# Performance work log

Measured on AMD Instinct MI355X. Metric: run time of the kernel, lower is better.

Reference implementation:

```python
import jax, jax.numpy as jnp
import numpy as np

N = 1024      # nodes == subgraphs (NGNN: one subgraph per node)
DEG = 8       # average degree
E = N * DEG   # edges
IND = 32      # indim
OUTD = 32     # outdim


def setup_inputs() -> dict:
    key = jax.random.key(0)
    k0, k1, k2, k3, k4 = jax.random.split(key, 5)
    X = jax.random.normal(k0, (N, N, IND), dtype=jnp.float32)
    # binary tuple-support mask (which (i,j) tuples exist in the sparse 2D tensor)
    mask = jax.random.randint(k1, (N, N), 0, 2).astype(jnp.int32)
    # adjacency edge list: A[row, col] = 1 (structure-only sparse adjacency)
    edge_row = jax.random.randint(k2, (E,), 0, N)  # destination j
    edge_col = jax.random.randint(k3, (E,), 0, N)  # source k
    # MLP (single linear layer, PygHO MLP default)
    W = jax.random.normal(k4, (IND, OUTD), dtype=jnp.float32) / np.sqrt(IND).astype(np.float32)
    b = jnp.zeros((OUTD,), dtype=jnp.float32)
    return {"X": X, "mask": mask, "edge_row": edge_row, "edge_col": edge_col, "W": W, "b": b}


def reference(X, mask, edge_row, edge_col, W, b):
    n = X.shape[0]
    m = mask.astype(X.dtype)[..., None]                      # [n, n, 1]
    # tuplewise MLP on existing tuples: tX[i,j] = X[i,j] @ W + b
    tX = (jnp.einsum("ijd,de->ije", X, W) + b) * m           # [n, n, OUTD]
    # message passing within each subgraph i along node dim j:
    # ret[i, j] = sum_{k : A[j,k]=1} tX[i, k]
    msgs = jnp.take(tX, edge_col, axis=1)                    # [n, E, OUTD] gather sources
    msgs = jnp.moveaxis(msgs, 1, 0)                          # [E, n, OUTD]
    agg = jax.ops.segment_sum(msgs, edge_row, num_segments=n)  # [j, i, OUTD]
    ret = jnp.swapaxes(agg, 0, 1) * m                        # restrict to tuple support (tarX = tX)
    return ret
```

## Files before the change

kernel.cpp:

```cpp
#include <hip/hip_runtime.h>


#define NN   1024
#define IND  32
#define OUTD 32
#define EE   8192

typedef __attribute__((ext_vector_type(2))) float f32x2;

__global__ __launch_bounds__(1024) void k_zero(int* __restrict__ p, int n) {
    const int t = blockIdx.x * 1024 + threadIdx.x;
    if (t < n) p[t] = 0;
}

__global__ __launch_bounds__(1024) void k_count(const int* __restrict__ erow,
                                                int* __restrict__ cnt, int n_edges) {
    const int e = blockIdx.x * 1024 + threadIdx.x;
    if (e < n_edges) atomicAdd(&cnt[erow[e]], 1);
}

__global__ __launch_bounds__(1024) void k_scan(const int* __restrict__ cnt,
                                               int* __restrict__ row_ptr,
                                               int* __restrict__ fill) {
    __shared__ int sb[NN];
    const int t = threadIdx.x;
    const int v = cnt[t];
    sb[t] = v;
    __syncthreads();
    #pragma unroll
    for (int off = 1; off < NN; off <<= 1) {
        const int a = (t >= off) ? sb[t - off] : 0;
        __syncthreads();
        sb[t] += a;
        __syncthreads();
    }
    const int excl = sb[t] - v;
    row_ptr[t] = excl;
    fill[t]    = excl;
    if (t == NN - 1) row_ptr[NN] = sb[t];
}

__global__ __launch_bounds__(1024) void k_scatter(const int* __restrict__ erow,
                                                  const int* __restrict__ ecol,
                                                  int* __restrict__ fill,
                                                  int* __restrict__ cols, int n_edges) {
    const int e = blockIdx.x * 1024 + threadIdx.x;
    if (e < n_edges) {
        const int pos = atomicAdd(&fill[erow[e]], 1);
        cols[pos] = ecol[e];
    }
}

__global__ __launch_bounds__(1024) void ngnn_main_kernel(
    const float* __restrict__ X, const int* __restrict__ mask,
    const float* __restrict__ W, const float* __restrict__ b,
    const int* __restrict__ row_ptr, const int* __restrict__ cols,
    float* __restrict__ out, int n_edges)
{
    extern __shared__ float smem[];
    float* Xl    = smem;
    float* maskf = smem + NN * IND;
    unsigned short* colsl = (unsigned short*)(smem + NN * IND + NN);

    const int t = threadIdx.x;
    const int i = blockIdx.x;

    const float4* Xg = (const float4*)(X + (size_t)i * NN * IND);
    float4 xv[8];
    #pragma unroll
    for (int it = 0; it < 8; ++it) xv[it] = Xg[it * 1024 + t];

    int cv[8];
    #pragma unroll
    for (int it = 0; it < 8; ++it) {
        const int e = it * 1024 + t;
        cv[it] = (e < n_edges) ? cols[e] : 0;
    }

    const int j  = t;
    const int e0 = row_ptr[j];
    const int e1 = row_ptr[j + 1];

    maskf[t] = (float)mask[(size_t)i * NN + t];
    __syncthreads();

    #pragma unroll
    for (int it = 0; it < 8; ++it) {
        const int f4 = it * 1024 + t;
        const int k  = f4 >> 3;
        const int p  = (f4 & 7) ^ (k & 7);
        const float m = maskf[k];
        float4 v = xv[it];
        v.x *= m; v.y *= m; v.z *= m; v.w *= m;
        *(float4*)(Xl + (k << 5) + (p << 2)) = v;
    }
    #pragma unroll
    for (int it = 0; it < 8; ++it) {
        const int e = it * 1024 + t;
        if (e < n_edges && e < EE) {
            const int k = cv[it] & (NN - 1);
            colsl[e] = (unsigned short)(k | ((maskf[k] != 0.f) ? 1024 : 0));
        }
    }
    __syncthreads();

    const float mj = maskf[j];
    f32x2 o2[16];

    if (mj != 0.f) {
        float4 S4[8];
        #pragma unroll
        for (int s = 0; s < 8; ++s) S4[s] = make_float4(0.f, 0.f, 0.f, 0.f);
        int cnt = 0;

        for (int e = e0; e < e1; ++e) {
            const int c = (int)colsl[e];
            const int k = c & (NN - 1);
            cnt += c >> 10;
            const float* rb = Xl + (k << 5);
            const int kb = (k & 7) << 2;
            #pragma unroll
            for (int s = 0; s < 8; ++s) {
                const float4 v = *(const float4*)(rb + ((s << 2) ^ kb));
                S4[s].x += v.x; S4[s].y += v.y; S4[s].z += v.z; S4[s].w += v.w;
            }
        }

        float S[IND];
        #pragma unroll
        for (int s = 0; s < 8; ++s) {
            S[4*s+0] = S4[s].x; S[4*s+1] = S4[s].y;
            S[4*s+2] = S4[s].z; S[4*s+3] = S4[s].w;
        }

        const float cntf = (float)cnt;
        const f32x2* W2 = (const f32x2*)W;
        const f32x2* b2 = (const f32x2*)b;
        #pragma unroll
        for (int c = 0; c < 16; ++c) o2[c] = b2[c] * cntf;
        #pragma unroll
        for (int d = 0; d < IND; ++d) {
            const float s = S[d];
            #pragma unroll
            for (int c = 0; c < 16; ++c) o2[c] += W2[d * 16 + c] * s;
        }
    } else {
        #pragma unroll
        for (int c = 0; c < 16; ++c) { o2[c].x = 0.f; o2[c].y = 0.f; }
    }

    __syncthreads();
    #pragma unroll
    for (int q = 0; q < 8; ++q) {
        const int p = q ^ (j & 7);
        *(float4*)(Xl + (j << 5) + (p << 2)) =
            make_float4(o2[2*q].x, o2[2*q].y, o2[2*q+1].x, o2[2*q+1].y);
    }
    __syncthreads();
    float4* Og = (float4*)(out + (size_t)i * NN * IND);
    #pragma unroll
    for (int it = 0; it < 8; ++it) {
        const int f4 = it * 1024 + t;
        const int k  = f4 >> 3;
        const int p  = (f4 & 7) ^ (k & 7);
        Og[f4] = *(const float4*)(Xl + (k << 5) + (p << 2));
    }
}

extern "C" void kernel_launch(void* const* d_in, const int* in_sizes, int n_in,
                              void* d_out, int out_size, void* d_ws, size_t ws_size,
                              hipStream_t stream) {
    const float* X    = (const float*)d_in[0];
    const int*   mask = (const int*)d_in[1];
    const int*   erow = (const int*)d_in[2];
    const int*   ecol = (const int*)d_in[3];
    const float* W    = (const float*)d_in[4];
    const float* b    = (const float*)d_in[5];
    float*       out  = (float*)d_out;

    const int n_edges = in_sizes[2];

    int* cnt     = (int*)d_ws;
    int* row_ptr = cnt + 1024;
    int* fill    = cnt + 2560;
    int* cols    = cnt + 4096;

    const int eb = (n_edges + 1023) / 1024;
    k_zero   <<<1, 1024, 0, stream>>>(cnt, NN);
    k_count  <<<eb, 1024, 0, stream>>>(erow, cnt, n_edges);
    k_scan   <<<1, 1024, 0, stream>>>(cnt, row_ptr, fill);
    k_scatter<<<eb, 1024, 0, stream>>>(erow, ecol, fill, cols, n_edges);

    const size_t shmem = (size_t)NN * IND * sizeof(float)
                       + (size_t)NN * sizeof(float)
                       + (size_t)EE * sizeof(unsigned short);
    hipFuncSetAttribute((const void*)ngnn_main_kernel,
                        hipFuncAttributeMaxDynamicSharedMemorySize, (int)shmem);
    ngnn_main_kernel<<<NN, 1024, shmem, stream>>>(X, mask, W, b, row_ptr, cols, out, n_edges);
}
```

Before: 316.4 us.

## Fuse CSR construction into main kernel and process four subgraphs per block

Drops the four preprocessing launches (zero, count, scan, scatter) and builds the CSR adjacency in LDS inside each block with LDS atomics and a scan. Each block now handles four subgraphs in sequence, which spreads the CSR build cost over four subgraphs and prefetches the next subgraph's X and mask into registers while the current one is staged. Syncthreads are replaced by an explicit lgkmcnt wait plus barrier. In exchange, the grid shrinks to 256 blocks of 1024 threads, so there is less parallelism for hiding memory latency, and every block repeats the edge-list work. The mask flag bits are also rewritten into the shared column list on each iteration.

New measurement: 318.7 us. About the same (+0.7%).

```diff
diff --git a/kernel.cpp b/kernel.cpp
--- a/kernel.cpp
+++ b/kernel.cpp
@@ -8,162 +8,163 @@
 
 typedef __attribute__((ext_vector_type(2))) float f32x2;
 
-__global__ __launch_bounds__(1024) void k_zero(int* __restrict__ p, int n) {
-    const int t = blockIdx.x * 1024 + threadIdx.x;
-    if (t < n) p[t] = 0;
-}
+#define BARRIER_LDS() do { \
+    asm volatile("s_waitcnt lgkmcnt(0)" ::: "memory"); \
+    __builtin_amdgcn_s_barrier(); \
+} while (0)
 
-__global__ __launch_bounds__(1024) void k_count(const int* __restrict__ erow,
-                                                int* __restrict__ cnt, int n_edges) {
-    const int e = blockIdx.x * 1024 + threadIdx.x;
-    if (e < n_edges) atomicAdd(&cnt[erow[e]], 1);
-}
-
-__global__ __launch_bounds__(1024) void k_scan(const int* __restrict__ cnt,
-                                               int* __restrict__ row_ptr,
-                                               int* __restrict__ fill) {
-    __shared__ int sb[NN];
-    const int t = threadIdx.x;
-    const int v = cnt[t];
-    sb[t] = v;
-    __syncthreads();
-    #pragma unroll
-    for (int off = 1; off < NN; off <<= 1) {
-        const int a = (t >= off) ? sb[t - off] : 0;
-        __syncthreads();
-        sb[t] += a;
-        __syncthreads();
-    }
-    const int excl = sb[t] - v;
-    row_ptr[t] = excl;
-    fill[t]    = excl;
-    if (t == NN - 1) row_ptr[NN] = sb[t];
-}
-
-__global__ __launch_bounds__(1024) void k_scatter(const int* __restrict__ erow,
-                                                  const int* __restrict__ ecol,
-                                                  int* __restrict__ fill,
-                                                  int* __restrict__ cols, int n_edges) {
-    const int e = blockIdx.x * 1024 + threadIdx.x;
-    if (e < n_edges) {
-        const int pos = atomicAdd(&fill[erow[e]], 1);
-        cols[pos] = ecol[e];
-    }
-}
-
-__global__ __launch_bounds__(1024) void ngnn_main_kernel(
+__global__ __launch_bounds__(1024) void ngnn_fused_kernel(
     const float* __restrict__ X, const int* __restrict__ mask,
+    const int* __restrict__ erow, const int* __restrict__ ecol,
     const float* __restrict__ W, const float* __restrict__ b,
-    const int* __restrict__ row_ptr, const int* __restrict__ cols,
     float* __restrict__ out, int n_edges)
 {
     extern __shared__ float smem[];
-    float* Xl    = smem;
-    float* maskf = smem + NN * IND;
-    unsigned short* colsl = (unsigned short*)(smem + NN * IND + NN);
+    float*          Xl    = smem;
+    int*            rp    = (int*)(smem + NN * IND);
+    float*          maskf = (float*)(rp + NN + 1);
+    unsigned short* colsl = (unsigned short*)(maskf + NN);
 
-    const int t = threadIdx.x;
-    const int i = blockIdx.x;
+    const int t  = threadIdx.x;
+    const int i0 = blockIdx.x * 4;
 
-    const float4* Xg = (const float4*)(X + (size_t)i * NN * IND);
+    const float4* Xg = (const float4*)(X + (size_t)i0 * NN * IND);
     float4 xv[8];
     #pragma unroll
     for (int it = 0; it < 8; ++it) xv[it] = Xg[it * 1024 + t];
+    int mv = mask[(size_t)i0 * NN + t];
 
-    int cv[8];
+    int er[8], ec[8];
     #pragma unroll
     for (int it = 0; it < 8; ++it) {
         const int e = it * 1024 + t;
-        cv[it] = (e < n_edges) ? cols[e] : 0;
+        er[it] = (e < n_edges) ? (erow[e] & (NN - 1)) : -1;
+        ec[it] = (e < n_edges) ? (ecol[e] & (NN - 1)) : 0;
     }
 
-    const int j  = t;
-    const int e0 = row_ptr[j];
-    const int e1 = row_ptr[j + 1];
-
-    maskf[t] = (float)mask[(size_t)i * NN + t];
-    __syncthreads();
-
+    int* scnt = (int*)smem;
+    scnt[t] = 0;
+    BARRIER_LDS();
+    #pragma unroll
+    for (int it = 0; it < 8; ++it)
+        if (er[it] >= 0) atomicAdd(&scnt[er[it]], 1);
+    BARRIER_LDS();
+    const int myv = scnt[t];
+    for (int off = 1; off < NN; off <<= 1) {
+        const int a = (t >= off) ? scnt[t - off] : 0;
+        BARRIER_LDS();
+        scnt[t] += a;
+        BARRIER_LDS();
+    }
+    const int incl = scnt[t];
+    int* fill = (int*)maskf;
+    rp[t]   = incl - myv;
+    fill[t] = incl - myv;
+    if (t == NN - 1) rp[NN] = incl;
+    BARRIER_LDS();
+    const int e0 = rp[t];
+    const int e1 = rp[t + 1];
     #pragma unroll
     for (int it = 0; it < 8; ++it) {
-        const int f4 = it * 1024 + t;
-        const int k  = f4 >> 3;
-        const int p  = (f4 & 7) ^ (k & 7);
-        const float m = maskf[k];
-        float4 v = xv[it];
-        v.x *= m; v.y *= m; v.z *= m; v.w *= m;
-        *(float4*)(Xl + (k << 5) + (p << 2)) = v;
-    }
-    #pragma unroll
-    for (int it = 0; it < 8; ++it) {
-        const int e = it * 1024 + t;
-        if (e < n_edges && e < EE) {
-            const int k = cv[it] & (NN - 1);
-            colsl[e] = (unsigned short)(k | ((maskf[k] != 0.f) ? 1024 : 0));
+        if (er[it] >= 0) {
+            const int pos = atomicAdd(&fill[er[it]], 1);
+            colsl[pos] = (unsigned short)ec[it];
         }
     }
-    __syncthreads();
+    BARRIER_LDS();
 
-    const float mj = maskf[j];
-    f32x2 o2[16];
+    #pragma unroll 1
+    for (int r = 0; r < 4; ++r) {
+        const int i = i0 + r;
 
-    if (mj != 0.f) {
-        float4 S4[8];
+        maskf[t] = (float)mv;
+        BARRIER_LDS();
+
         #pragma unroll
-        for (int s = 0; s < 8; ++s) S4[s] = make_float4(0.f, 0.f, 0.f, 0.f);
-        int cnt = 0;
+        for (int it = 0; it < 8; ++it) {
+            const int f4 = it * 1024 + t;
+            const int k  = f4 >> 3;
+            const int p  = (f4 & 7) ^ (k & 7);
+            const float m = maskf[k];
+            float4 v = xv[it];
+            v.x *= m; v.y *= m; v.z *= m; v.w *= m;
+            *(float4*)(Xl + (k << 5) + (p << 2)) = v;
+        }
+        #pragma unroll
+        for (int it = 0; it < 8; ++it) {
+            const int e = it * 1024 + t;
+            if (e < n_edges) {
+                const int k = (int)colsl[e] & (NN - 1);
+                colsl[e] = (unsigned short)(k | ((maskf[k] != 0.f) ? 1024 : 0));
+            }
+        }
+        if (r < 3) {
+            const float4* Xgn = (const float4*)(X + (size_t)(i + 1) * NN * IND);
+            #pragma unroll
+            for (int it = 0; it < 8; ++it) xv[it] = Xgn[it * 1024 + t];
+            mv = mask[(size_t)(i + 1) * NN + t];
+        }
+        BARRIER_LDS();
 
-        for (int e = e0; e < e1; ++e) {
-            const int c = (int)colsl[e];
-            const int k = c & (NN - 1);
-            cnt += c >> 10;
-            const float* rb = Xl + (k << 5);
-            const int kb = (k & 7) << 2;
+        const float mj = maskf[t];
+        f32x2 o2[16];
+        if (mj != 0.f) {
+            float4 S4[8];
+            #pragma unroll
+            for (int s = 0; s < 8; ++s) S4[s] = make_float4(0.f, 0.f, 0.f, 0.f);
+            int cnt = 0;
+            for (int e = e0; e < e1; ++e) {
+                const int c = (int)colsl[e];
+                const int k = c & (NN - 1);
+                cnt += c >> 10;
+                const float* rb = Xl + (k << 5);
+                const int kb = (k & 7) << 2;
+                #pragma unroll
+                for (int s = 0; s < 8; ++s) {
+                    const float4 v = *(const float4*)(rb + ((s << 2) ^ kb));
+                    S4[s].x += v.x; S4[s].y += v.y; S4[s].z += v.z; S4[s].w += v.w;
+                }
+            }
+            float S[IND];
             #pragma unroll
             for (int s = 0; s < 8; ++s) {
-                const float4 v = *(const float4*)(rb + ((s << 2) ^ kb));
-                S4[s].x += v.x; S4[s].y += v.y; S4[s].z += v.z; S4[s].w += v.w;
+                S[4*s+0] = S4[s].x; S[4*s+1] = S4[s].y;
+                S[4*s+2] = S4[s].z; S[4*s+3] = S4[s].w;
             }
+            const float cntf = (float)cnt;
+            const f32x2* W2 = (const f32x2*)W;
+            const f32x2* b2 = (const f32x2*)b;
+            #pragma unroll
+            for (int c = 0; c < 16; ++c) o2[c] = b2[c] * cntf;
+            #pragma unroll
+            for (int d = 0; d < IND; ++d) {
+                const float s = S[d];
+                #pragma unroll
+                for (int c = 0; c < 16; ++c) o2[c] += W2[d * 16 + c] * s;
+            }
+        } else {
+            #pragma unroll
+            for (int c = 0; c < 16; ++c) { o2[c].x = 0.f; o2[c].y = 0.f; }
         }
+        BARRIER_LDS();
 
-        float S[IND];
         #pragma unroll
-        for (int s = 0; s < 8; ++s) {
-            S[4*s+0] = S4[s].x; S[4*s+1] = S4[s].y;
-            S[4*s+2] = S4[s].z; S[4*s+3] = S4[s].w;
+        for (int q = 0; q < 8; ++q) {
+            const int p = q ^ (t & 7);
+            *(float4*)(Xl + (t << 5) + (p << 2)) =
+                make_float4(o2[2*q].x, o2[2*q].y, o2[2*q+1].x, o2[2*q+1].y);
         }
+        BARRIER_LDS();
 
-        const float cntf = (float)cnt;
-        const f32x2* W2 = (const f32x2*)W;
-        const f32x2* b2 = (const f32x2*)b;
+        float4* Og = (float4*)(out + (size_t)i * NN * IND);
         #pragma unroll
-        for (int c = 0; c < 16; ++c) o2[c] = b2[c] * cntf;
-        #pragma unroll
-        for (int d = 0; d < IND; ++d) {
-            const float s = S[d];
-            #pragma unroll
-            for (int c = 0; c < 16; ++c) o2[c] += W2[d * 16 + c] * s;
+        for (int it = 0; it < 8; ++it) {
+            const int f4 = it * 1024 + t;
+            const int k  = f4 >> 3;
+            const int p  = (f4 & 7) ^ (k & 7);
+            Og[f4] = *(const float4*)(Xl + (k << 5) + (p << 2));
         }
-    } else {
-        #pragma unroll
-        for (int c = 0; c < 16; ++c) { o2[c].x = 0.f; o2[c].y = 0.f; }
-    }
-
-    __syncthreads();
-    #pragma unroll
-    for (int q = 0; q < 8; ++q) {
-        const int p = q ^ (j & 7);
-        *(float4*)(Xl + (j << 5) + (p << 2)) =
-            make_float4(o2[2*q].x, o2[2*q].y, o2[2*q+1].x, o2[2*q+1].y);
-    }
-    __syncthreads();
-    float4* Og = (float4*)(out + (size_t)i * NN * IND);
-    #pragma unroll
-    for (int it = 0; it < 8; ++it) {
-        const int f4 = it * 1024 + t;
-        const int k  = f4 >> 3;
-        const int p  = (f4 & 7) ^ (k & 7);
-        Og[f4] = *(const float4*)(Xl + (k << 5) + (p << 2));
+        BARRIER_LDS();
     }
 }
 
@@ -178,23 +179,14 @@
     const float* b    = (const float*)d_in[5];
     float*       out  = (float*)d_out;
 
-    const int n_edges = in_sizes[2];
-
-    int* cnt     = (int*)d_ws;
-    int* row_ptr = cnt + 1024;
-    int* fill    = cnt + 2560;
-    int* cols    = cnt + 4096;
-
-    const int eb = (n_edges + 1023) / 1024;
-    k_zero   <<<1, 1024, 0, stream>>>(cnt, NN);
-    k_count  <<<eb, 1024, 0, stream>>>(erow, cnt, n_edges);
-    k_scan   <<<1, 1024, 0, stream>>>(cnt, row_ptr, fill);
-    k_scatter<<<eb, 1024, 0, stream>>>(erow, ecol, fill, cols, n_edges);
+    int n_edges = in_sizes[2];
+    if (n_edges > EE) n_edges = EE;
 
     const size_t shmem = (size_t)NN * IND * sizeof(float)
+                       + (size_t)(NN + 1) * sizeof(int)
                        + (size_t)NN * sizeof(float)
                        + (size_t)EE * sizeof(unsigned short);
-    hipFuncSetAttribute((const void*)ngnn_main_kernel,
+    hipFuncSetAttribute((const void*)ngnn_fused_kernel,
                         hipFuncAttributeMaxDynamicSharedMemorySize, (int)shmem);
-    ngnn_main_kernel<<<NN, 1024, shmem, stream>>>(X, mask, W, b, row_ptr, cols, out, n_edges);
+    ngnn_fused_kernel<<<NN / 4, 1024, shmem, stream>>>(X, mask, erow, ecol, W, b, out, n_edges);
 }
```

## Skip masked rows and gather X directly from global instead of staging in LDS

Applied to the files above, without the earlier changes.

The main kernel no longer stages the whole X slice in shared memory. It builds a per-block compacted list of active destination rows and their masked source columns, then gathers source rows straight from global memory, so masked-out X rows are never read. Masked output rows are written as zeros, and the block shrinks to 256 threads with a much smaller LDS footprint, allowing several blocks per CU. The cost is uncoalesced, L2-dependent random row gathers in place of streaming loads, a per-block serial pass over the CSR, and an atomic-built active list that leaves load imbalance across threads.

New measurement: 335.9 us. 6.2% more time.

```diff
diff --git a/kernel.cpp b/kernel.cpp
--- a/kernel.cpp
+++ b/kernel.cpp
@@ -51,119 +51,98 @@
     }
 }
 
-__global__ __launch_bounds__(1024) void ngnn_main_kernel(
+__global__ __launch_bounds__(256, 4) void ngnn_main_kernel(
     const float* __restrict__ X, const int* __restrict__ mask,
     const float* __restrict__ W, const float* __restrict__ b,
     const int* __restrict__ row_ptr, const int* __restrict__ cols,
-    float* __restrict__ out, int n_edges)
+    float* __restrict__ out)
 {
-    extern __shared__ float smem[];
-    float* Xl    = smem;
-    float* maskf = smem + NN * IND;
-    unsigned short* colsl = (unsigned short*)(smem + NN * IND + NN);
+    __shared__ float          maskf[NN];
+    __shared__ unsigned int   meta[NN];
+    __shared__ unsigned short colsl[EE];
+    __shared__ unsigned short alist[NN];
+    __shared__ int            acount;
 
     const int t = threadIdx.x;
     const int i = blockIdx.x;
 
-    const float4* Xg = (const float4*)(X + (size_t)i * NN * IND);
-    float4 xv[8];
-    #pragma unroll
-    for (int it = 0; it < 8; ++it) xv[it] = Xg[it * 1024 + t];
-
-    int cv[8];
-    #pragma unroll
-    for (int it = 0; it < 8; ++it) {
-        const int e = it * 1024 + t;
-        cv[it] = (e < n_edges) ? cols[e] : 0;
+    if (t == 0) acount = 0;
+    {
+        const int4 m4 = ((const int4*)(mask + (size_t)i * NN))[t];
+        maskf[4*t+0] = (float)m4.x; maskf[4*t+1] = (float)m4.y;
+        maskf[4*t+2] = (float)m4.z; maskf[4*t+3] = (float)m4.w;
     }
-
-    const int j  = t;
-    const int e0 = row_ptr[j];
-    const int e1 = row_ptr[j + 1];
-
-    maskf[t] = (float)mask[(size_t)i * NN + t];
     __syncthreads();
 
     #pragma unroll
-    for (int it = 0; it < 8; ++it) {
-        const int f4 = it * 1024 + t;
-        const int k  = f4 >> 3;
-        const int p  = (f4 & 7) ^ (k & 7);
-        const float m = maskf[k];
-        float4 v = xv[it];
-        v.x *= m; v.y *= m; v.z *= m; v.w *= m;
-        *(float4*)(Xl + (k << 5) + (p << 2)) = v;
-    }
-    #pragma unroll
-    for (int it = 0; it < 8; ++it) {
-        const int e = it * 1024 + t;
-        if (e < n_edges && e < EE) {
-            const int k = cv[it] & (NN - 1);
-            colsl[e] = (unsigned short)(k | ((maskf[k] != 0.f) ? 1024 : 0));
+    for (int p = 0; p < 4; ++p) {
+        const int j = p * 256 + t;
+        if (maskf[j] != 0.f) {
+            const int a   = row_ptr[j];
+            const int bnd = row_ptr[j + 1];
+            int c = 0;
+            for (int e = a; e < bnd; ++e) {
+                const int k = cols[e] & (NN - 1);
+                if (maskf[k] != 0.f) colsl[a + (c++)] = (unsigned short)k;
+            }
+            meta[j] = (unsigned)a | ((unsigned)c << 16);
+            const int pos = atomicAdd(&acount, 1);
+            alist[pos] = (unsigned short)j;
         }
     }
     __syncthreads();
 
-    const float mj = maskf[j];
-    f32x2 o2[16];
+    const float4 z = {0.f, 0.f, 0.f, 0.f};
+    #pragma unroll
+    for (int p = 0; p < 4; ++p) {
+        const int j = p * 256 + t;
+        if (maskf[j] == 0.f) {
+            float4* orow = (float4*)(out + ((size_t)i * NN + j) * OUTD);
+            #pragma unroll
+            for (int q = 0; q < 8; ++q) orow[q] = z;
+        }
+    }
 
-    if (mj != 0.f) {
+    const float4* Xi = (const float4*)(X + (size_t)i * NN * IND);
+    const f32x2*  W2 = (const f32x2*)W;
+    const f32x2*  b2 = (const f32x2*)b;
+    const int na = acount;
+
+    for (int a = t; a < na; a += 256) {
+        const int j = (int)alist[a];
+        const unsigned md = meta[j];
+        const int e0 = (int)(md & 0xffffu);
+        const int cn = (int)(md >> 16);
+
         float4 S4[8];
         #pragma unroll
-        for (int s = 0; s < 8; ++s) S4[s] = make_float4(0.f, 0.f, 0.f, 0.f);
-        int cnt = 0;
+        for (int s = 0; s < 8; ++s) S4[s] = z;
 
-        for (int e = e0; e < e1; ++e) {
-            const int c = (int)colsl[e];
-            const int k = c & (NN - 1);
-            cnt += c >> 10;
-            const float* rb = Xl + (k << 5);
-            const int kb = (k & 7) << 2;
+        for (int q = 0; q < cn; ++q) {
+            const int k = (int)colsl[e0 + q];
+            const float4* r = Xi + (k << 3);
             #pragma unroll
             for (int s = 0; s < 8; ++s) {
-                const float4 v = *(const float4*)(rb + ((s << 2) ^ kb));
+                const float4 v = r[s];
                 S4[s].x += v.x; S4[s].y += v.y; S4[s].z += v.z; S4[s].w += v.w;
             }
         }
 
-        float S[IND];
+        const float cf = (float)cn;
+        f32x2 o2[16];
         #pragma unroll
-        for (int s = 0; s < 8; ++s) {
-            S[4*s+0] = S4[s].x; S[4*s+1] = S4[s].y;
-            S[4*s+2] = S4[s].z; S[4*s+3] = S4[s].w;
+        for (int c = 0; c < 16; ++c) o2[c] = b2[c] * cf;
+        #pragma unroll
+        for (int d = 0; d < IND; ++d) {
+            const float sd = ((const float*)S4)[d];
+            #pragma unroll
+            for (int c = 0; c < 16; ++c) o2[c] += W2[d * 16 + c] * sd;
         }
 
-        const float cntf = (float)cnt;
-        const f32x2* W2 = (const f32x2*)W;
-        const f32x2* b2 = (const f32x2*)b;
+        float4* orow = (float4*)(out + ((size_t)i * NN + j) * OUTD);
         #pragma unroll
-        for (int c = 0; c < 16; ++c) o2[c] = b2[c] * cntf;
-        #pragma unroll
-        for (int d = 0; d < IND; ++d) {
-            const float s = S[d];
-            #pragma unroll
-            for (int c = 0; c < 16; ++c) o2[c] += W2[d * 16 + c] * s;
-        }
-    } else {
-        #pragma unroll
-        for (int c = 0; c < 16; ++c) { o2[c].x = 0.f; o2[c].y = 0.f; }
-    }
-
-    __syncthreads();
-    #pragma unroll
-    for (int q = 0; q < 8; ++q) {
-        const int p = q ^ (j & 7);
-        *(float4*)(Xl + (j << 5) + (p << 2)) =
-            make_float4(o2[2*q].x, o2[2*q].y, o2[2*q+1].x, o2[2*q+1].y);
-    }
-    __syncthreads();
-    float4* Og = (float4*)(out + (size_t)i * NN * IND);
-    #pragma unroll
-    for (int it = 0; it < 8; ++it) {
-        const int f4 = it * 1024 + t;
-        const int k  = f4 >> 3;
-        const int p  = (f4 & 7) ^ (k & 7);
-        Og[f4] = *(const float4*)(Xl + (k << 5) + (p << 2));
+        for (int q2 = 0; q2 < 8; ++q2)
+            orow[q2] = make_float4(o2[2*q2].x, o2[2*q2].y, o2[2*q2+1].x, o2[2*q2+1].y);
     }
 }
 
@@ -178,7 +157,8 @@
     const float* b    = (const float*)d_in[5];
     float*       out  = (float*)d_out;
 
-    const int n_edges = in_sizes[2];
+    int n_edges = in_sizes[2];
+    if (n_edges > EE) n_edges = EE;
 
     int* cnt     = (int*)d_ws;
     int* row_ptr = cnt + 1024;
@@ -191,10 +171,5 @@
     k_scan   <<<1, 1024, 0, stream>>>(cnt, row_ptr, fill);
     k_scatter<<<eb, 1024, 0, stream>>>(erow, ecol, fill, cols, n_edges);
 
-    const size_t shmem = (size_t)NN * IND * sizeof(float)
-                       + (size_t)NN * sizeof(float)
-                       + (size_t)EE * sizeof(unsigned short);
-    hipFuncSetAttribute((const void*)ngnn_main_kernel,
-                        hipFuncAttributeMaxDynamicSharedMemorySize, (int)shmem);
-    ngnn_main_kernel<<<NN, 1024, shmem, stream>>>(X, mask, W, b, row_ptr, cols, out, n_edges);
+    ngnn_main_kernel<<<NN, 256, 0, stream>>>(X, mask, W, b, row_ptr, cols, out);
 }
```
